# Optimization experiments

Measured on AMD Instinct MI355X. Metric: run time of the kernel, lower is better.

Reference implementation:

```python
import jax, jax.numpy as jnp
import numpy as np

B = 32
H = 56
WD = 56
C = 192
NH = 6
WS = 7   # window size
SS = 3   # shift size
HID = 4 * C
N = WS * WS
NW = (H // WS) * (WD // WS)


def _rel_pos_index():
    coords = np.stack(np.meshgrid(np.arange(WS), np.arange(WS), indexing='ij'))  # [2,ws,ws]
    cf = coords.reshape(2, -1)
    rel = cf[:, :, None] - cf[:, None, :]          # [2,N,N]
    rel = rel.transpose(1, 2, 0)
    rel[..., 0] += WS - 1
    rel[..., 1] += WS - 1
    rel[..., 0] *= 2 * WS - 1
    return rel.sum(-1)                              # [N,N] int


def _attn_mask():
    img = np.zeros((H, WD))
    sl = (slice(0, -WS), slice(-WS, -SS), slice(-SS, None))
    cnt = 0
    for hs in sl:
        for ws in sl:
            img[hs, ws] = cnt
            cnt += 1
    mw = img.reshape(H // WS, WS, WD // WS, WS).transpose(0, 2, 1, 3).reshape(-1, N)  # [nW,N]
    d = mw[:, None, :] - mw[:, :, None]
    return np.where(d != 0, -100.0, 0.0).astype(np.float32)  # [nW,N,N]


_RPI = jnp.asarray(_rel_pos_index())
_MASK = jnp.asarray(_attn_mask())


def setup_inputs() -> dict:
    key = jax.random.key(0)
    ks = jax.random.split(key, 8)
    s = 0.02
    return {
        'x': jax.random.normal(ks[0], (B, H * WD, C), jnp.float32),
        'norm1_g': jnp.ones((C,), jnp.float32),
        'norm1_b': jnp.zeros((C,), jnp.float32),
        'qkv_w': jax.random.normal(ks[1], (C, 3 * C), jnp.float32) * s,
        'qkv_b': jnp.zeros((3 * C,), jnp.float32),
        'rel_bias': jax.random.normal(ks[2], ((2 * WS - 1) ** 2, NH), jnp.float32) * s,
        'proj_w': jax.random.normal(ks[3], (C, C), jnp.float32) * s,
        'proj_b': jnp.zeros((C,), jnp.float32),
        'norm2_g': jnp.ones((C,), jnp.float32),
        'norm2_b': jnp.zeros((C,), jnp.float32),
        'fc1_w': jax.random.normal(ks[4], (C, HID), jnp.float32) * s,
        'fc1_b': jnp.zeros((HID,), jnp.float32),
        'fc2_w': jax.random.normal(ks[5], (HID, C), jnp.float32) * s,
        'fc2_b': jnp.zeros((C,), jnp.float32),
    }


def _ln(x, g, b, eps=1e-5):
    m = jnp.mean(x, axis=-1, keepdims=True)
    v = jnp.mean(jnp.square(x - m), axis=-1, keepdims=True)
    return (x - m) / jnp.sqrt(v + eps) * g + b


def reference(x, norm1_g, norm1_b, qkv_w, qkv_b, rel_bias, proj_w, proj_b,
              norm2_g, norm2_b, fc1_w, fc1_b, fc2_w, fc2_b):
    hd = C // NH
    shortcut = x
    xn = _ln(x, norm1_g, norm1_b).reshape(B, H, WD, C)
    xs = jnp.roll(xn, (-SS, -SS), axis=(1, 2))                     # cyclic shift
    # window partition -> [B*nW, N, C]
    xw = xs.reshape(B, H // WS, WS, WD // WS, WS, C)
    xw = xw.transpose(0, 1, 3, 2, 4, 5).reshape(-1, N, C)
    # windowed attention
    qkv = (xw @ qkv_w + qkv_b).reshape(-1, N, 3, NH, hd).transpose(2, 0, 3, 1, 4)
    q, k, v = qkv[0], qkv[1], qkv[2]                               # [B*nW, NH, N, hd]
    attn = jnp.einsum('whnd,whmd->whnm', q * (hd ** -0.5), k)      # [B*nW, NH, N, N]
    bias = rel_bias[_RPI.reshape(-1)].reshape(N, N, NH).transpose(2, 0, 1)
    attn = attn + bias[None]
    attn = attn.reshape(B, NW, NH, N, N) + _MASK[None, :, None]
    attn = jax.nn.softmax(attn.reshape(-1, NH, N, N), axis=-1)
    out = jnp.einsum('whnm,whmd->whnd', attn, v)
    out = out.transpose(0, 2, 1, 3).reshape(-1, N, C)
    out = out @ proj_w + proj_b
    # window reverse + un-shift
    out = out.reshape(B, H // WS, WD // WS, WS, WS, C)
    out = out.transpose(0, 1, 3, 2, 4, 5).reshape(B, H, WD, C)
    out = jnp.roll(out, (SS, SS), axis=(1, 2)).reshape(B, H * WD, C)
    x = shortcut + out
    # MLP (exact GELU, matching torch nn.GELU default)
    xm = _ln(x, norm2_g, norm2_b)
    h = jax.nn.gelu(xm @ fc1_w + fc1_b, approximate=False)
    return x + (h @ fc2_w + fc2_b)
```

## Files before the change

kernel.cpp:

```cpp
#include <hip/hip_runtime.h>
#include <math.h>


constexpr long T = 100352;

typedef __attribute__((ext_vector_type(8))) short short8;
typedef __attribute__((ext_vector_type(4))) float f32x4;

__device__ __forceinline__ short bf16(float f) {
    union { float f; unsigned u; } v; v.f = f;
    return (short)((v.u + 0x7fff + ((v.u >> 16) & 1)) >> 16);
}

template<int K, int N>
__global__ __launch_bounds__(256)
void pack_k(const float* __restrict__ W, short* __restrict__ P)
{
    const int idx = blockIdx.x * 256 + threadIdx.x;
    const int k = idx / N, n = idx - k * N;
    constexpr int Kst = K / 32;
    const int flat = (((n >> 4) * Kst + (k >> 5)) * 64 +
                      (((k >> 3) & 3) << 4) + (n & 15)) * 8 + (k & 7);
    P[flat] = bf16(W[idx]);
}

__global__ __launch_bounds__(256)
void pack_fc2_k(const float* __restrict__ W, short* __restrict__ P)
{
    const int idx = blockIdx.x * 256 + threadIdx.x;
    const int k = idx / 192, n = idx - k * 192;
    const int t = k >> 6, ks = (k >> 5) & 1, nt = n >> 4;
    const int flat = ((((t * 12 + nt) << 1) + ks) * 64 +
                      (((k >> 3) & 3) << 4) + (n & 15)) * 8 + (k & 7);
    P[flat] = bf16(W[idx]);
}

__global__ __launch_bounds__(256)
void pack_proj_k(const float* __restrict__ W, short* __restrict__ P)
{
    const int idx = blockIdx.x * 256 + threadIdx.x;
    const int k = idx / 192, n = idx - k * 192;
    const int ks = k >> 5, nt = n >> 4;
    const int flat = (((ks * 12 + nt) * 64) +
                      (((k >> 3) & 3) << 4) + (n & 15)) * 8 + (k & 7);
    P[flat] = bf16(W[idx]);
}

__global__ __launch_bounds__(256)
void biasprep_k(const float* __restrict__ relb, float* __restrict__ bm)
{
    const int idx = blockIdx.x * 256 + threadIdx.x;
    if (idx >= 6 * 4 * 2401) return;
    const int e = idx % 2401, rest = idx / 2401;
    const int tw = rest & 1, th = (rest >> 1) & 1, head = rest >> 2;
    const int i = e / 49, j = e - i * 49;
    const int yi = i / 7, xi = i - yi * 7, yj = j / 7, xj = j - yj * 7;
    const float v = relb[((yi - yj + 6) * 13 + (xi - xj + 6)) * 6 + head];
    const int hi = th ? 49 + yi : yi, hj = th ? 49 + yj : yj;
    const int wa = tw ? 49 + xi : xi, wb = tw ? 49 + xj : xj;
    const int Li = (hi < 49 ? 0 : (hi < 53 ? 1 : 2)) * 3 + (wa < 49 ? 0 : (wa < 53 ? 1 : 2));
    const int Lj = (hj < 49 ? 0 : (hj < 53 ? 1 : 2)) * 3 + (wb < 49 ? 0 : (wb < 53 ? 1 : 2));
    bm[idx] = (Li != Lj) ? v - 100.0f : v;
}

__global__ __launch_bounds__(256)
void lnstats_k(const float* __restrict__ x, float* __restrict__ mean,
               float* __restrict__ rstd)
{
    const int wave = threadIdx.x >> 6;
    const int lane = threadIdx.x & 63;
    const long tok = (long)blockIdx.x * 4 + wave;
    const float* p = x + tok * 192;
    const float a = p[lane], b = p[lane + 64], c = p[lane + 128];
    float s = a + b + c;
    float q = a * a + b * b + c * c;
    #pragma unroll
    for (int off = 32; off > 0; off >>= 1) {
        s += __shfl_xor(s, off);
        q += __shfl_xor(q, off);
    }
    if (lane == 0) {
        const float m = s * (1.0f / 192.0f);
        const float v = q * (1.0f / 192.0f) - m * m;
        mean[tok] = m;
        rstd[tok] = 1.0f / sqrtf(v + 1e-5f);
    }
}

__global__ __launch_bounds__(256, 4)
void winattn_k(const float* __restrict__ x, const float* __restrict__ n1g,
               const float* __restrict__ n1b, const short* __restrict__ qkvP,
               const float* __restrict__ qkv_b, const float* __restrict__ bm,
               const float* __restrict__ mean, const float* __restrict__ rstd,
               float* __restrict__ outp)
{
    __shared__ __align__(16) short Kb[2][2048];
    __shared__ __align__(16) short Vb[2][2048];
    __shared__ __align__(16) short Pf[4][1024];
    const int bw  = blockIdx.x;
    const int tid = threadIdx.x;
    const int b = bw >> 6, wi = bw & 63, wh = wi >> 3, ww = wi & 7;
    const int wave = tid >> 6, lane = tid & 63;
    const int col = lane & 15, rbase = (lane >> 4) << 2;
    const float scale = 0.17677669529663687f;

    const int am = lane & 15;
    const int arow = (wave << 4) + am;
    const int kof = (lane >> 4) << 3;
    short8 afr[6];
    long tokA = 0; float mA = 0.f, rsA = 1.f;
    const bool avalid = arow < 49;
    if (avalid) {
        const int yi = arow / 7, xi = arow - yi * 7;
        int h = wh * 7 + yi + 3; if (h >= 56) h -= 56;
        int w = ww * 7 + xi + 3; if (w >= 56) w -= 56;
        tokA = (long)b * 3136 + h * 56 + w;
        mA = mean[tokA]; rsA = rstd[tokA];
    }
    #pragma unroll
    for (int ks = 0; ks < 6; ++ks) {
        short8 a = {};
        if (avalid) {
            const int k0 = (ks << 5) + kof;
            const float4 v0 = *(const float4*)(x + tokA * 192 + k0);
            const float4 v1 = *(const float4*)(x + tokA * 192 + k0 + 4);
            const float4 g0 = *(const float4*)(n1g + k0);
            const float4 g1 = *(const float4*)(n1g + k0 + 4);
            const float4 e0 = *(const float4*)(n1b + k0);
            const float4 e1 = *(const float4*)(n1b + k0 + 4);
            a[0] = bf16((v0.x - mA) * rsA * g0.x + e0.x);
            a[1] = bf16((v0.y - mA) * rsA * g0.y + e0.y);
            a[2] = bf16((v0.z - mA) * rsA * g0.z + e0.z);
            a[3] = bf16((v0.w - mA) * rsA * g0.w + e0.w);
            a[4] = bf16((v1.x - mA) * rsA * g1.x + e1.x);
            a[5] = bf16((v1.y - mA) * rsA * g1.y + e1.y);
            a[6] = bf16((v1.z - mA) * rsA * g1.z + e1.z);
            a[7] = bf16((v1.w - mA) * rsA * g1.w + e1.w);
        }
        afr[ks] = a;
    }

    short8 qfrag[6];
    #pragma unroll
    for (int nt = 0; nt < 12; ++nt) {
        f32x4 acc = {};
        #pragma unroll
        for (int ks = 0; ks < 6; ++ks) {
            const short8 bfr = *(const short8*)(qkvP + ((nt * 6 + ks) * 64 + lane) * 8);
            acc = __builtin_amdgcn_mfma_f32_16x16x32_bf16(afr[ks], bfr, acc, 0, 0, 0);
        }
        const int hh = nt >> 1, d = ((nt & 1) << 4) + col;
        const float bias = qkv_b[hh * 32 + d];
        #pragma unroll
        for (int r = 0; r < 4; ++r) {
            const int m = rbase + r;
            Pf[wave][((m + (((d >> 3) & 3) << 4)) << 3) + (d & 7)] =
                bf16((acc[r] + bias) * scale);
        }
        if (nt & 1) qfrag[hh] = *(const short8*)&Pf[wave][lane << 3];
    }

    long tok_r[4]; bool iv[4]; int i49[4];
    #pragma unroll
    for (int r = 0; r < 4; ++r) {
        const int i = (wave << 4) + rbase + r;
        iv[r] = i < 49;
        i49[r] = iv[r] ? i * 49 : 0;
        if (iv[r]) {
            const int yi = i / 7, xi = i - yi * 7;
            int h = wh * 7 + yi + 3; if (h >= 56) h -= 56;
            int w = ww * 7 + xi + 3; if (w >= 56) w -= 56;
            tok_r[r] = (long)b * 3136 + h * 56 + w;
        } else tok_r[r] = 0;
    }

    f32x4 oa[12] = {};

    for (int h = 0; h < 6; ++h) {
        const int bs = h & 1;
        #pragma unroll
        for (int half = 0; half < 2; ++half) {
            const int d = (half << 4) + col;
            f32x4 acck = {};
            #pragma unroll
            for (int ks = 0; ks < 6; ++ks) {
                const short8 bfr = *(const short8*)(qkvP +
                    (((12 + 2 * h + half) * 6 + ks) * 64 + lane) * 8);
                acck = __builtin_amdgcn_mfma_f32_16x16x32_bf16(afr[ks], bfr, acck, 0, 0, 0);
            }
            const float biask = qkv_b[192 + h * 32 + d];
            #pragma unroll
            for (int r = 0; r < 4; ++r) {
                const int m = rbase + r;
                Kb[bs][(((wave << 6) + m + (((d >> 3) & 3) << 4)) << 3) + (d & 7)] =
                    bf16(acck[r] + biask);
            }
            f32x4 accv = {};
            #pragma unroll
            for (int ks = 0; ks < 6; ++ks) {
                const short8 bfr = *(const short8*)(qkvP +
                    (((24 + 2 * h + half) * 6 + ks) * 64 + lane) * 8);
                accv = __builtin_amdgcn_mfma_f32_16x16x32_bf16(afr[ks], bfr, accv, 0, 0, 0);
            }
            const float biasv = qkv_b[384 + h * 32 + d];
            #pragma unroll
            for (int r = 0; r < 4; ++r) {
                const int m = rbase + r;
                const int flat = ((((half << 1) + (wave >> 1)) << 6) + col +
                                  ((((wave << 1) + (m >> 3)) & 3) << 4)) * 8 + (m & 7);
                Vb[bs][flat] = bf16(accv[r] + biasv);
            }
        }
        __syncthreads();

        const float* bmp = bm + (((h << 1) + (wh == 7)) * 2 + (ww == 7)) * 2401;
        f32x4 sa[4];
        #pragma unroll
        for (int jt = 0; jt < 4; ++jt) {
            f32x4 z = {};
            const short8 kfr = *(const short8*)&Kb[bs][((jt << 6) + lane) << 3];
            sa[jt] = __builtin_amdgcn_mfma_f32_16x16x32_bf16(qfrag[h], kfr, z, 0, 0, 0);
        }
        float p[4][4];
        #pragma unroll
        for (int jt = 0; jt < 4; ++jt) {
            const int j = (jt << 4) + col;
            #pragma unroll
            for (int r = 0; r < 4; ++r)
                p[jt][r] = (j < 49) ? sa[jt][r] + bmp[i49[r] + j] : -1e30f;
        }
        #pragma unroll
        for (int r = 0; r < 4; ++r) {
            float mx = fmaxf(fmaxf(p[0][r], p[1][r]), fmaxf(p[2][r], p[3][r]));
            mx = fmaxf(mx, __shfl_xor(mx, 1));
            mx = fmaxf(mx, __shfl_xor(mx, 2));
            mx = fmaxf(mx, __shfl_xor(mx, 4));
            mx = fmaxf(mx, __shfl_xor(mx, 8));
            float sum = 0.f;
            #pragma unroll
            for (int jt = 0; jt < 4; ++jt) {
                const float e = (((jt << 4) + col) < 49) ? __expf(p[jt][r] - mx) : 0.f;
                p[jt][r] = e; sum += e;
            }
            sum += __shfl_xor(sum, 1);
            sum += __shfl_xor(sum, 2);
            sum += __shfl_xor(sum, 4);
            sum += __shfl_xor(sum, 8);
            const float inv = 1.0f / sum;
            #pragma unroll
            for (int jt = 0; jt < 4; ++jt) p[jt][r] *= inv;
        }
        #pragma unroll
        for (int jt = 0; jt < 4; ++jt) {
            #pragma unroll
            for (int r = 0; r < 4; ++r) {
                const int m = rbase + r;
                const int flat = (((jt >> 1) << 6) + m +
                                  ((((jt & 1) << 1) + (col >> 3)) << 4)) * 8 + (col & 7);
                Pf[wave][flat] = bf16(p[jt][r]);
            }
        }
        const short8 p0 = *(const short8*)&Pf[wave][lane << 3];
        const short8 p1 = *(const short8*)&Pf[wave][(64 + lane) << 3];
        #pragma unroll
        for (int dt = 0; dt < 2; ++dt) {
            const short8 v0 = *(const short8*)&Vb[bs][(((dt << 1) << 6) + lane) << 3];
            const short8 v1 = *(const short8*)&Vb[bs][((((dt << 1) + 1) << 6) + lane) << 3];
            oa[h * 2 + dt] = __builtin_amdgcn_mfma_f32_16x16x32_bf16(p0, v0, oa[h * 2 + dt], 0, 0, 0);
            oa[h * 2 + dt] = __builtin_amdgcn_mfma_f32_16x16x32_bf16(p1, v1, oa[h * 2 + dt], 0, 0, 0);
        }
    }

    #pragma unroll
    for (int r = 0; r < 4; ++r) {
        if (!iv[r]) continue;
        float* op = outp + tok_r[r] * 192;
        #pragma unroll
        for (int hh = 0; hh < 6; ++hh) {
            op[hh * 32 + col]      = oa[hh * 2 + 0][r];
            op[hh * 32 + 16 + col] = oa[hh * 2 + 1][r];
        }
    }
}

__global__ __launch_bounds__(256, 2)
void projmlp_k(const float* attnb, const short* __restrict__ projP,
               const float* __restrict__ pb, const float* __restrict__ x,
               const float* __restrict__ n2g, const float* __restrict__ n2b,
               const short* __restrict__ fc1P, const float* __restrict__ b1,
               const short* __restrict__ fc2P, const float* __restrict__ b2,
               float* outp)
{
    __shared__ __align__(16) short S1[12288];
    __shared__ __align__(16) short S2[12288];
    __shared__ __align__(16) short Xf[12288];
    __shared__ __align__(16) short Hs[4096];
    const int tid = threadIdx.x;
    const int wave = tid >> 6, lane = tid & 63;
    const int col = lane & 15, rbase = (lane >> 4) << 2;
    const int kof = (lane >> 4) << 3;
    const long m0 = (long)blockIdx.x * 64;

    const long arow = m0 + (wave << 4) + col;
    const float* ap = attnb + arow * 192;
    short8 afr[6];
    #pragma unroll
    for (int ks = 0; ks < 6; ++ks) {
        const int k0 = (ks << 5) + kof;
        const float4 v0 = *(const float4*)(ap + k0);
        const float4 v1 = *(const float4*)(ap + k0 + 4);
        short8 a;
        a[0] = bf16(v0.x); a[1] = bf16(v0.y); a[2] = bf16(v0.z); a[3] = bf16(v0.w);
        a[4] = bf16(v1.x); a[5] = bf16(v1.y); a[6] = bf16(v1.z); a[7] = bf16(v1.w);
        afr[ks] = a;
    }
    f32x4 x1a[12] = {};
    #pragma unroll
    for (int ks = 0; ks < 6; ++ks) {
        #pragma unroll
        for (int nt = 0; nt < 12; ++nt) {
            const short8 bfr = *(const short8*)(projP + ks * 6144 + (nt << 9) + (lane << 3));
            x1a[nt] = __builtin_amdgcn_mfma_f32_16x16x32_bf16(afr[ks], bfr, x1a[nt], 0, 0, 0);
        }
    }
    const long orow = m0 + (wave << 4) + rbase;
    #pragma unroll
    for (int nt = 0; nt < 12; ++nt) {
        const int n = (nt << 4) + col;
        const float bias = pb[n];
        #pragma unroll
        for (int r = 0; r < 4; ++r)
            x1a[nt][r] += bias + x[(orow + r) * 192 + n];
    }
    float s0 = 0.f, s1_ = 0.f, s2_ = 0.f, s3 = 0.f;
    float q0 = 0.f, q1 = 0.f, q2 = 0.f, q3 = 0.f;
    #pragma unroll
    for (int nt = 0; nt < 12; ++nt) {
        s0 += x1a[nt][0]; q0 += x1a[nt][0] * x1a[nt][0];
        s1_ += x1a[nt][1]; q1 += x1a[nt][1] * x1a[nt][1];
        s2_ += x1a[nt][2]; q2 += x1a[nt][2] * x1a[nt][2];
        s3 += x1a[nt][3]; q3 += x1a[nt][3] * x1a[nt][3];
    }
    #pragma unroll
    for (int off = 8; off > 0; off >>= 1) {
        s0 += __shfl_xor(s0, off); q0 += __shfl_xor(q0, off);
        s1_ += __shfl_xor(s1_, off); q1 += __shfl_xor(q1, off);
        s2_ += __shfl_xor(s2_, off); q2 += __shfl_xor(q2, off);
        s3 += __shfl_xor(s3, off); q3 += __shfl_xor(q3, off);
    }
    float mr[4], rr[4];
    mr[0] = s0 * (1.0f / 192.0f); rr[0] = rsqrtf(q0 * (1.0f / 192.0f) - mr[0] * mr[0] + 1e-5f);
    mr[1] = s1_ * (1.0f / 192.0f); rr[1] = rsqrtf(q1 * (1.0f / 192.0f) - mr[1] * mr[1] + 1e-5f);
    mr[2] = s2_ * (1.0f / 192.0f); rr[2] = rsqrtf(q2 * (1.0f / 192.0f) - mr[2] * mr[2] + 1e-5f);
    mr[3] = s3 * (1.0f / 192.0f); rr[3] = rsqrtf(q3 * (1.0f / 192.0f) - mr[3] * mr[3] + 1e-5f);
    short* Xw = Xf + wave * 3072;
    #pragma unroll
    for (int nt = 0; nt < 12; ++nt) {
        const int k = (nt << 4) + col;
        const float g = n2g[k], bb = n2b[k];
        #pragma unroll
        for (int r = 0; r < 4; ++r) {
            const int row16 = rbase + r;
            const int flat = (((k >> 5) << 6) + (((k >> 3) & 3) << 4) + row16) * 8 + (k & 7);
            Xw[flat] = bf16((x1a[nt][r] - mr[r]) * rr[r] * g + bb);
        }
    }

    const short8* f1p = (const short8*)fc1P;
    const short8* f2p = (const short8*)fc2P;
    short8 R1[6], R2[6];
    #pragma unroll
    for (int i = 0; i < 6; ++i) {
        R1[i] = f1p[tid + (i << 8)];
        R2[i] = f2p[tid + (i << 8)];
    }
    short* Hw = Hs + wave * 1024;
    f32x4 accO[12] = {};
    for (int t = 0; t < 12; ++t) {
        __syncthreads();
        #pragma unroll
        for (int i = 0; i < 6; ++i) {
            ((short8*)S1)[tid + (i << 8)] = R1[i];
            ((short8*)S2)[tid + (i << 8)] = R2[i];
        }
        __syncthreads();
        if (t < 11) {
            const short8* n1p = f1p + (t + 1) * 1536;
            const short8* n2p = f2p + (t + 1) * 1536;
            #pragma unroll
            for (int i = 0; i < 6; ++i) {
                R1[i] = n1p[tid + (i << 8)];
                R2[i] = n2p[tid + (i << 8)];
            }
        }
        f32x4 accH[4] = {};
        #pragma unroll
        for (int ks = 0; ks < 6; ++ks) {
            const short8 a = *(const short8*)(Xw + (((ks << 6) + lane) << 3));
            #pragma unroll
            for (int nt = 0; nt < 4; ++nt) {
                const short8 bfr = *(const short8*)&S1[((nt * 6 + ks) << 9) + (lane << 3)];
                accH[nt] = __builtin_amdgcn_mfma_f32_16x16x32_bf16(a, bfr, accH[nt], 0, 0, 0);
            }
        }
        #pragma unroll
        for (int nt = 0; nt < 4; ++nt) {
            const int kh = (nt << 4) + col;
            const float bias = b1[(t << 6) + kh];
            #pragma unroll
            for (int r = 0; r < 4; ++r) {
                const int m = rbase + r;
                float val = accH[nt][r] + bias;
                val = 0.5f * val * (1.0f + erff(val * 0.7071067811865476f));
                const int flat = (((kh >> 5) << 6) + (((kh >> 3) & 3) << 4) + m) * 8 + (kh & 7);
                Hw[flat] = bf16(val);
            }
        }
        #pragma unroll
        for (int ks = 0; ks < 2; ++ks) {
            const short8 a = *(const short8*)(Hw + (((ks << 6) + lane) << 3));
            #pragma unroll
            for (int nt = 0; nt < 12; ++nt) {
                const short8 bfr = *(const short8*)&S2[(((nt << 1) + ks) << 9) + (lane << 3)];
                accO[nt] = __builtin_amdgcn_mfma_f32_16x16x32_bf16(a, bfr, accO[nt], 0, 0, 0);
            }
        }
    }

    #pragma unroll
    for (int nt = 0; nt < 12; ++nt) {
        const int n = (nt << 4) + col;
        const float bias = b2[n];
        #pragma unroll
        for (int r = 0; r < 4; ++r)
            outp[(orow + r) * 192 + n] = accO[nt][r] + bias + x1a[nt][r];
    }
}

extern "C" void kernel_launch(void* const* d_in, const int* in_sizes, int n_in,
                              void* d_out, int out_size, void* d_ws, size_t ws_size,
                              hipStream_t stream)
{
    const float* x      = (const float*)d_in[0];
    const float* n1g    = (const float*)d_in[1];
    const float* n1b    = (const float*)d_in[2];
    const float* qkv_w  = (const float*)d_in[3];
    const float* qkv_b  = (const float*)d_in[4];
    const float* relb   = (const float*)d_in[5];
    const float* proj_w = (const float*)d_in[6];
    const float* proj_b = (const float*)d_in[7];
    const float* n2g    = (const float*)d_in[8];
    const float* n2b    = (const float*)d_in[9];
    const float* fc1_w  = (const float*)d_in[10];
    const float* fc1_b  = (const float*)d_in[11];
    const float* fc2_w  = (const float*)d_in[12];
    const float* fc2_b  = (const float*)d_in[13];
    float* out = (float*)d_out;
    char*  ws  = (char*)d_ws;

    float* mb    = (float*)(ws);
    float* rb    = (float*)(ws +   401408L);
    short* qkvP  = (short*)(ws +   802816L);
    short* projP = (short*)(ws +  1024000L);
    short* fc1P  = (short*)(ws +  1097728L);
    short* fc2P  = (short*)(ws +  1392640L);
    float* bmT   = (float*)(ws +  1687552L);

    pack_k<192, 576><<<432, 256, 0, stream>>>(qkv_w, qkvP);
    pack_proj_k<<<144, 256, 0, stream>>>(proj_w, projP);
    pack_k<192, 768><<<576, 256, 0, stream>>>(fc1_w, fc1P);
    pack_fc2_k<<<576, 256, 0, stream>>>(fc2_w, fc2P);
    biasprep_k<<<226, 256, 0, stream>>>(relb, bmT);

    lnstats_k<<<T / 4, 256, 0, stream>>>(x, mb, rb);
    winattn_k<<<2048, 256, 0, stream>>>(x, n1g, n1b, qkvP, qkv_b,
                                        bmT, mb, rb, out);
    projmlp_k<<<T / 64, 256, 0, stream>>>(out, projP, proj_b, x, n2g, n2b,
                                          fc1P, fc1_b, fc2P, fc2_b, out);
}
```

Before: 524.2 us.

## Merge prep kernels and cut projmlp LDS/registers for higher occupancy

Merges the five weight-pack and bias-prep kernels plus the LN-stats kernel into a single prep launch, removing several launch gaps. In the projmlp kernel, the normalized-activation tile now reuses the S1 buffer and is held in registers. The per-wave hidden buffer is halved by interleaving GELU and the fc2 MFMAs per 32-wide half. Weight tiles are loaded straight into LDS with global_load_lds instead of being register-prefetched. Together these shrink LDS and register use so launch bounds can rise to 3 blocks per CU, at the cost of losing the overlap from the previous register-level prefetch of the next weight tile.

After: 519.1 us. No clear change (-1.0%).

```diff
diff --git a/kernel.cpp b/kernel.cpp
--- a/kernel.cpp
+++ b/kernel.cpp
@@ -12,78 +12,80 @@
     return (short)((v.u + 0x7fff + ((v.u >> 16) & 1)) >> 16);
 }
 
-template<int K, int N>
+__device__ __forceinline__ void gll16(const void* g, void* l) {
+    __builtin_amdgcn_global_load_lds(
+        (const __attribute__((address_space(1))) void*)g,
+        (__attribute__((address_space(3))) void*)l, 16, 0, 0);
+}
+
 __global__ __launch_bounds__(256)
-void pack_k(const float* __restrict__ W, short* __restrict__ P)
+void prep_k(const float* __restrict__ qkv_w, const float* __restrict__ proj_w,
+            const float* __restrict__ fc1_w, const float* __restrict__ fc2_w,
+            const float* __restrict__ relb, const float* __restrict__ x,
+            short* __restrict__ qkvP, short* __restrict__ projP,
+            short* __restrict__ fc1P, short* __restrict__ fc2P,
+            float* __restrict__ bm, float* __restrict__ mean,
+            float* __restrict__ rstd)
 {
-    const int idx = blockIdx.x * 256 + threadIdx.x;
-    const int k = idx / N, n = idx - k * N;
-    constexpr int Kst = K / 32;
-    const int flat = (((n >> 4) * Kst + (k >> 5)) * 64 +
-                      (((k >> 3) & 3) << 4) + (n & 15)) * 8 + (k & 7);
-    P[flat] = bf16(W[idx]);
-}
-
-__global__ __launch_bounds__(256)
-void pack_fc2_k(const float* __restrict__ W, short* __restrict__ P)
-{
-    const int idx = blockIdx.x * 256 + threadIdx.x;
-    const int k = idx / 192, n = idx - k * 192;
-    const int t = k >> 6, ks = (k >> 5) & 1, nt = n >> 4;
-    const int flat = ((((t * 12 + nt) << 1) + ks) * 64 +
-                      (((k >> 3) & 3) << 4) + (n & 15)) * 8 + (k & 7);
-    P[flat] = bf16(W[idx]);
-}
-
-__global__ __launch_bounds__(256)
-void pack_proj_k(const float* __restrict__ W, short* __restrict__ P)
-{
-    const int idx = blockIdx.x * 256 + threadIdx.x;
-    const int k = idx / 192, n = idx - k * 192;
-    const int ks = k >> 5, nt = n >> 4;
-    const int flat = (((ks * 12 + nt) * 64) +
-                      (((k >> 3) & 3) << 4) + (n & 15)) * 8 + (k & 7);
-    P[flat] = bf16(W[idx]);
-}
-
-__global__ __launch_bounds__(256)
-void biasprep_k(const float* __restrict__ relb, float* __restrict__ bm)
-{
-    const int idx = blockIdx.x * 256 + threadIdx.x;
-    if (idx >= 6 * 4 * 2401) return;
-    const int e = idx % 2401, rest = idx / 2401;
-    const int tw = rest & 1, th = (rest >> 1) & 1, head = rest >> 2;
-    const int i = e / 49, j = e - i * 49;
-    const int yi = i / 7, xi = i - yi * 7, yj = j / 7, xj = j - yj * 7;
-    const float v = relb[((yi - yj + 6) * 13 + (xi - xj + 6)) * 6 + head];
-    const int hi = th ? 49 + yi : yi, hj = th ? 49 + yj : yj;
-    const int wa = tw ? 49 + xi : xi, wb = tw ? 49 + xj : xj;
-    const int Li = (hi < 49 ? 0 : (hi < 53 ? 1 : 2)) * 3 + (wa < 49 ? 0 : (wa < 53 ? 1 : 2));
-    const int Lj = (hj < 49 ? 0 : (hj < 53 ? 1 : 2)) * 3 + (wb < 49 ? 0 : (wb < 53 ? 1 : 2));
-    bm[idx] = (Li != Lj) ? v - 100.0f : v;
-}
-
-__global__ __launch_bounds__(256)
-void lnstats_k(const float* __restrict__ x, float* __restrict__ mean,
-               float* __restrict__ rstd)
-{
-    const int wave = threadIdx.x >> 6;
-    const int lane = threadIdx.x & 63;
-    const long tok = (long)blockIdx.x * 4 + wave;
-    const float* p = x + tok * 192;
-    const float a = p[lane], b = p[lane + 64], c = p[lane + 128];
-    float s = a + b + c;
-    float q = a * a + b * b + c * c;
-    #pragma unroll
-    for (int off = 32; off > 0; off >>= 1) {
-        s += __shfl_xor(s, off);
-        q += __shfl_xor(q, off);
-    }
-    if (lane == 0) {
-        const float m = s * (1.0f / 192.0f);
-        const float v = q * (1.0f / 192.0f) - m * m;
-        mean[tok] = m;
-        rstd[tok] = 1.0f / sqrtf(v + 1e-5f);
+    const int bid = blockIdx.x;
+    const int tid = threadIdx.x;
+    if (bid < 432) {
+        const int idx = bid * 256 + tid;
+        const int k = idx / 576, n = idx - k * 576;
+        const int flat = (((n >> 4) * 6 + (k >> 5)) * 64 +
+                          (((k >> 3) & 3) << 4) + (n & 15)) * 8 + (k & 7);
+        qkvP[flat] = bf16(qkv_w[idx]);
+    } else if (bid < 576) {
+        const int idx = (bid - 432) * 256 + tid;
+        const int k = idx / 192, n = idx - k * 192;
+        const int flat = ((((k >> 5) * 12 + (n >> 4)) * 64) +
+                          (((k >> 3) & 3) << 4) + (n & 15)) * 8 + (k & 7);
+        projP[flat] = bf16(proj_w[idx]);
+    } else if (bid < 1152) {
+        const int idx = (bid - 576) * 256 + tid;
+        const int k = idx / 768, n = idx - k * 768;
+        const int flat = (((n >> 4) * 6 + (k >> 5)) * 64 +
+                          (((k >> 3) & 3) << 4) + (n & 15)) * 8 + (k & 7);
+        fc1P[flat] = bf16(fc1_w[idx]);
+    } else if (bid < 1728) {
+        const int idx = (bid - 1152) * 256 + tid;
+        const int k = idx / 192, n = idx - k * 192;
+        const int t = k >> 6, ks = (k >> 5) & 1, nt = n >> 4;
+        const int flat = ((((t * 12 + nt) << 1) + ks) * 64 +
+                          (((k >> 3) & 3) << 4) + (n & 15)) * 8 + (k & 7);
+        fc2P[flat] = bf16(fc2_w[idx]);
+    } else if (bid < 1954) {
+        const int idx = (bid - 1728) * 256 + tid;
+        if (idx >= 6 * 4 * 2401) return;
+        const int e = idx % 2401, rest = idx / 2401;
+        const int tw = rest & 1, th = (rest >> 1) & 1, head = rest >> 2;
+        const int i = e / 49, j = e - i * 49;
+        const int yi = i / 7, xi = i - yi * 7, yj = j / 7, xj = j - yj * 7;
+        const float v = relb[((yi - yj + 6) * 13 + (xi - xj + 6)) * 6 + head];
+        const int hi = th ? 49 + yi : yi, hj = th ? 49 + yj : yj;
+        const int wa = tw ? 49 + xi : xi, wb = tw ? 49 + xj : xj;
+        const int Li = (hi < 49 ? 0 : (hi < 53 ? 1 : 2)) * 3 + (wa < 49 ? 0 : (wa < 53 ? 1 : 2));
+        const int Lj = (hj < 49 ? 0 : (hj < 53 ? 1 : 2)) * 3 + (wb < 49 ? 0 : (wb < 53 ? 1 : 2));
+        bm[idx] = (Li != Lj) ? v - 100.0f : v;
+    } else {
+        const int wave = tid >> 6;
+        const int lane = tid & 63;
+        const long tok = (long)(bid - 1954) * 4 + wave;
+        const float* p = x + tok * 192;
+        const float a = p[lane], b = p[lane + 64], c = p[lane + 128];
+        float s = a + b + c;
+        float q = a * a + b * b + c * c;
+        #pragma unroll
+        for (int off = 32; off > 0; off >>= 1) {
+            s += __shfl_xor(s, off);
+            q += __shfl_xor(q, off);
+        }
+        if (lane == 0) {
+            const float m = s * (1.0f / 192.0f);
+            const float v = q * (1.0f / 192.0f) - m * m;
+            mean[tok] = m;
+            rstd[tok] = 1.0f / sqrtf(v + 1e-5f);
+        }
     }
 }
 
@@ -283,7 +285,7 @@
     }
 }
 
-__global__ __launch_bounds__(256, 2)
+__global__ __launch_bounds__(256, 3)
 void projmlp_k(const float* attnb, const short* __restrict__ projP,
                const float* __restrict__ pb, const float* __restrict__ x,
                const float* __restrict__ n2g, const float* __restrict__ n2b,
@@ -293,8 +295,7 @@
 {
     __shared__ __align__(16) short S1[12288];
     __shared__ __align__(16) short S2[12288];
-    __shared__ __align__(16) short Xf[12288];
-    __shared__ __align__(16) short Hs[4096];
+    __shared__ __align__(16) short Hs[2048];
     const int tid = threadIdx.x;
     const int wave = tid >> 6, lane = tid & 63;
     const int col = lane & 15, rbase = (lane >> 4) << 2;
@@ -353,7 +354,8 @@
     mr[1] = s1_ * (1.0f / 192.0f); rr[1] = rsqrtf(q1 * (1.0f / 192.0f) - mr[1] * mr[1] + 1e-5f);
     mr[2] = s2_ * (1.0f / 192.0f); rr[2] = rsqrtf(q2 * (1.0f / 192.0f) - mr[2] * mr[2] + 1e-5f);
     mr[3] = s3 * (1.0f / 192.0f); rr[3] = rsqrtf(q3 * (1.0f / 192.0f) - mr[3] * mr[3] + 1e-5f);
-    short* Xw = Xf + wave * 3072;
+
+    short* Xw = S1 + wave * 3072;
     #pragma unroll
     for (int nt = 0; nt < 12; ++nt) {
         const int k = (nt << 4) + col;
@@ -365,64 +367,56 @@
             Xw[flat] = bf16((x1a[nt][r] - mr[r]) * rr[r] * g + bb);
         }
     }
-
-    const short8* f1p = (const short8*)fc1P;
-    const short8* f2p = (const short8*)fc2P;
-    short8 R1[6], R2[6];
-    #pragma unroll
-    for (int i = 0; i < 6; ++i) {
-        R1[i] = f1p[tid + (i << 8)];
-        R2[i] = f2p[tid + (i << 8)];
-    }
-    short* Hw = Hs + wave * 1024;
+    short8 afrX[6];
+    #pragma unroll
+    for (int ks = 0; ks < 6; ++ks)
+        afrX[ks] = *(const short8*)(Xw + (((ks << 6) + lane) << 3));
+
+    short* Hw = Hs + wave * 512;
     f32x4 accO[12] = {};
     for (int t = 0; t < 12; ++t) {
         __syncthreads();
-        #pragma unroll
-        for (int i = 0; i < 6; ++i) {
-            ((short8*)S1)[tid + (i << 8)] = R1[i];
-            ((short8*)S2)[tid + (i << 8)] = R2[i];
+        {
+            const short* f1 = fc1P + t * 12288;
+            const short* f2 = fc2P + t * 12288;
+            #pragma unroll
+            for (int i = 0; i < 6; ++i) {
+                const int slot = (i << 8) + (wave << 6);
+                gll16(f1 + ((slot + lane) << 3), S1 + (slot << 3));
+                gll16(f2 + ((slot + lane) << 3), S2 + (slot << 3));
+            }
         }
         __syncthreads();
-        if (t < 11) {
-            const short8* n1p = f1p + (t + 1) * 1536;
-            const short8* n2p = f2p + (t + 1) * 1536;
-            #pragma unroll
-            for (int i = 0; i < 6; ++i) {
-                R1[i] = n1p[tid + (i << 8)];
-                R2[i] = n2p[tid + (i << 8)];
-            }
-        }
         f32x4 accH[4] = {};
         #pragma unroll
         for (int ks = 0; ks < 6; ++ks) {
-            const short8 a = *(const short8*)(Xw + (((ks << 6) + lane) << 3));
             #pragma unroll
             for (int nt = 0; nt < 4; ++nt) {
                 const short8 bfr = *(const short8*)&S1[((nt * 6 + ks) << 9) + (lane << 3)];
-                accH[nt] = __builtin_amdgcn_mfma_f32_16x16x32_bf16(a, bfr, accH[nt], 0, 0, 0);
-            }
-        }
-        #pragma unroll
-        for (int nt = 0; nt < 4; ++nt) {
-            const int kh = (nt << 4) + col;
-            const float bias = b1[(t << 6) + kh];
-            #pragma unroll
-            for (int r = 0; r < 4; ++r) {
-                const int m = rbase + r;
-                float val = accH[nt][r] + bias;
-                val = 0.5f * val * (1.0f + erff(val * 0.7071067811865476f));
-                const int flat = (((kh >> 5) << 6) + (((kh >> 3) & 3) << 4) + m) * 8 + (kh & 7);
-                Hw[flat] = bf16(val);
-            }
-        }
-        #pragma unroll
-        for (int ks = 0; ks < 2; ++ks) {
-            const short8 a = *(const short8*)(Hw + (((ks << 6) + lane) << 3));
-            #pragma unroll
-            for (int nt = 0; nt < 12; ++nt) {
-                const short8 bfr = *(const short8*)&S2[(((nt << 1) + ks) << 9) + (lane << 3)];
-                accO[nt] = __builtin_amdgcn_mfma_f32_16x16x32_bf16(a, bfr, accO[nt], 0, 0, 0);
+                accH[nt] = __builtin_amdgcn_mfma_f32_16x16x32_bf16(afrX[ks], bfr, accH[nt], 0, 0, 0);
+            }
+        }
+        #pragma unroll
+        for (int hf = 0; hf < 2; ++hf) {
+            #pragma unroll
+            for (int ntl = 0; ntl < 2; ++ntl) {
+                const int nt = (hf << 1) + ntl;
+                const int kh = (nt << 4) + col;
+                const float bias = b1[(t << 6) + kh];
+                #pragma unroll
+                for (int r = 0; r < 4; ++r) {
+                    const int m = rbase + r;
+                    float val = accH[nt][r] + bias;
+                    val = 0.5f * val * (1.0f + erff(val * 0.7071067811865476f));
+                    const int flat = ((((kh >> 3) & 3) << 4) + m) * 8 + (kh & 7);
+                    Hw[flat] = bf16(val);
+                }
+            }
+            const short8 a = *(const short8*)(Hw + (lane << 3));
+            #pragma unroll
+            for (int nt2 = 0; nt2 < 12; ++nt2) {
+                const short8 bfr = *(const short8*)&S2[(((nt2 << 1) + hf) << 9) + (lane << 3)];
+                accO[nt2] = __builtin_amdgcn_mfma_f32_16x16x32_bf16(a, bfr, accO[nt2], 0, 0, 0);
             }
         }
     }
@@ -466,13 +460,9 @@
     short* fc2P  = (short*)(ws +  1392640L);
     float* bmT   = (float*)(ws +  1687552L);
 
-    pack_k<192, 576><<<432, 256, 0, stream>>>(qkv_w, qkvP);
-    pack_proj_k<<<144, 256, 0, stream>>>(proj_w, projP);
-    pack_k<192, 768><<<576, 256, 0, stream>>>(fc1_w, fc1P);
-    pack_fc2_k<<<576, 256, 0, stream>>>(fc2_w, fc2P);
-    biasprep_k<<<226, 256, 0, stream>>>(relb, bmT);
-
-    lnstats_k<<<T / 4, 256, 0, stream>>>(x, mb, rb);
+    prep_k<<<1954 + T / 4, 256, 0, stream>>>(qkv_w, proj_w, fc1_w, fc2_w,
+                                             relb, x, qkvP, projP, fc1P,
+                                             fc2P, bmT, mb, rb);
     winattn_k<<<2048, 256, 0, stream>>>(x, n1g, n1b, qkvP, qkv_b,
                                         bmT, mb, rb, out);
     projmlp_k<<<T / 64, 256, 0, stream>>>(out, projP, proj_b, x, n2g, n2b,
```
